# Kernel optimization log

Hardware: AMD Instinct MI355X
Metric: run time of the kernel (lower is better)

Reference implementation:

```python
import jax, jax.numpy as jnp
import numpy as np

B, A, D = 16384, 16, 256  # batch, n_different_edges (= attribute nodes), embedding_size


def setup_inputs() -> dict:
    key = jax.random.key(0)
    k0, k1, k2, k3, k4 = jax.random.split(key, 5)
    image_features = jax.random.normal(k0, (B, D), jnp.float32)
    edge_attributes = jax.random.normal(k1, (B, A, D), jnp.float32)
    # Linear(2D -> D): torch stores weight as [out, in]
    W_agg = jax.random.normal(k2, (D, 2 * D), jnp.float32) / np.sqrt(2 * D)
    b_agg = jnp.zeros((D,), jnp.float32)
    # per-edge-type projection matrices (kaiming-uniform in torch; scaled normal here)
    P_fwd = jax.random.normal(k3, (A, D, D), jnp.float32) * np.sqrt(2.0 / D)
    P_bwd = jax.random.normal(k4, (A, D, D), jnp.float32) * np.sqrt(2.0 / D)
    self_weighted = jnp.ones((1, A, 1), jnp.float32)
    return {
        "image_features": image_features,
        "edge_attributes": edge_attributes,
        "W_agg": W_agg,
        "b_agg": b_agg,
        "P_fwd": P_fwd,
        "P_bwd": P_bwd,
        "self_weighted": self_weighted,
    }


def reference(image_features, edge_attributes, W_agg, b_agg, P_fwd, P_bwd, self_weighted):
    b, a, d = edge_attributes.shape
    # ForwardAttributeGnn: broadcast src over attribute nodes, concat, Linear, per-edge-type bmm
    src = jnp.broadcast_to(image_features[:, None, :], (b, a, d))
    cat = jnp.concatenate([src, edge_attributes], axis=-1)          # [B, A, 2D]
    agg = jnp.einsum('bak,ok->bao', cat, W_agg) + b_agg             # Linear(2D->D)
    attribute_representation = jnp.einsum('bai,aij->baj', agg, P_fwd)  # [B, A, D]
    # BackwardAttributeGnn: per-edge-type bmm, ReLU, weighted sum over attribute axis
    proj = jax.nn.relu(jnp.einsum('bai,aij->baj', attribute_representation, P_bwd))
    individual_embeddings = jnp.sum(proj * self_weighted, axis=1)   # [B, D]
    return attribute_representation, individual_embeddings
```

## Files before the change

### kernel.cpp

```cpp
#include <hip/hip_runtime.h>
#include <hip/hip_bf16.h>


typedef __bf16 bf16_t;
typedef __bf16 bf16x4 __attribute__((ext_vector_type(4)));
typedef __bf16 bf16x8 __attribute__((ext_vector_type(8)));
typedef float f32x4 __attribute__((ext_vector_type(4)));

#define NB 16384
#define NA 16
#define ND 256
#define BM 64

__device__ __forceinline__ int swz(int r, int c) {
    return r * 256 + (c ^ ((r & 15) << 3));
}

__device__ __forceinline__ bf16x8 cvt8(f32x4 a, f32x4 b) {
    bf16x8 r;
    r[0] = (bf16_t)a.x; r[1] = (bf16_t)a.y; r[2] = (bf16_t)a.z; r[3] = (bf16_t)a.w;
    r[4] = (bf16_t)b.x; r[5] = (bf16_t)b.y; r[6] = (bf16_t)b.z; r[7] = (bf16_t)b.w;
    return r;
}

__global__ void prep_wfrag(const float* __restrict__ W,
                           bf16_t* __restrict__ W1f, bf16_t* __restrict__ W2f)
{
    int t = blockIdx.x * 256 + threadIdx.x;
    int lane = t & 63;
    int ks = (t >> 6) & 7;
    int nt = (t >> 9) & 15;
    int half = t >> 13;
    int row = nt * 16 + (lane & 15);
    int col = ks * 32 + (lane >> 4) * 8;
    const float* src = W + (size_t)row * 512 + half * 256 + col;
    bf16_t* dst = (half ? W2f : W1f) + ((nt * 8 + ks) * 64 + lane) * 8;
    bf16x8 v;
#pragma unroll
    for (int m = 0; m < 8; ++m) v[m] = (bf16_t)src[m];
    *(bf16x8*)dst = v;
}

__global__ void prep_pfrag2(const float* __restrict__ Pf, const float* __restrict__ Pb,
                            bf16_t* __restrict__ Pff, bf16_t* __restrict__ Pbf)
{
    int gw = (blockIdx.x * 256 + threadIdx.x) >> 6;
    int lane = threadIdx.x & 63;
    int frag = gw & 127;
    int a = (gw >> 7) & 15;
    int mat = gw >> 11;
    int nt = frag >> 3, ks = frag & 7;
    const float* src = (mat ? Pb : Pf) + (size_t)a * 65536;
    bf16_t* dst = (mat ? Pbf : Pff) + (size_t)a * 65536 + ((size_t)frag * 64 + lane) * 8;
    int i0 = ks * 32 + (lane >> 4) * 8;
    int j = nt * 16 + (lane & 15);
    bf16x8 v;
#pragma unroll
    for (int m = 0; m < 8; ++m)
        v[m] = (bf16_t)src[(size_t)(i0 + m) * 256 + j];
    *(bf16x8*)dst = v;
}

__global__ __launch_bounds__(512, 2)
void fused_main(const float* __restrict__ img, const float* __restrict__ bias,
                const float* __restrict__ edge,
                const bf16_t* __restrict__ W1f, const bf16_t* __restrict__ W2f,
                const bf16_t* __restrict__ Pff, const bf16_t* __restrict__ Pbf,
                const float* __restrict__ sw, float* __restrict__ out)
{
    __shared__ bf16_t EG[BM * 256];
    __shared__ bf16_t Rl[BM * 256];
    __shared__ float  Tl[BM * 256];

    const int tid = threadIdx.x;
    const int lane = tid & 63;
    const int wc = tid >> 6;
    const int lr = lane & 15;
    const int lhi = lane >> 4;
    const int brow0 = blockIdx.x * BM;
    const int sr = tid >> 3;
    const int scb = (tid & 7) * 32;

    bf16x8 B[2][8];

#define LOADB(MAT) do {                                                       \
    const bf16_t* bp_ = (MAT) + (size_t)wc * 16 * 512 + lane * 8;             \
    _Pragma("unroll") for (int ni_ = 0; ni_ < 2; ++ni_)                       \
    _Pragma("unroll") for (int ks_ = 0; ks_ < 8; ++ks_)                       \
        B[ni_][ks_] = *(const bf16x8*)&bp_[(ni_ * 8 + ks_) * 512];            \
} while (0)

#define SUBGEMM(SRC, IB, ACC) do {                                            \
    _Pragma("unroll") for (int ks_ = 0; ks_ < 8; ++ks_) {                     \
        const int kc_ = ks_ * 32 + lhi * 8;                                   \
        bf16x8 af0_ = *(const bf16x8*)&(SRC)[swz((IB) * 32 + lr, kc_)];       \
        bf16x8 af1_ = *(const bf16x8*)&(SRC)[swz((IB) * 32 + 16 + lr, kc_)];  \
        ACC[0][0] = __builtin_amdgcn_mfma_f32_16x16x32_bf16(af0_, B[0][ks_], ACC[0][0], 0, 0, 0); \
        ACC[1][0] = __builtin_amdgcn_mfma_f32_16x16x32_bf16(af1_, B[0][ks_], ACC[1][0], 0, 0, 0); \
        ACC[0][1] = __builtin_amdgcn_mfma_f32_16x16x32_bf16(af0_, B[1][ks_], ACC[0][1], 0, 0, 0); \
        ACC[1][1] = __builtin_amdgcn_mfma_f32_16x16x32_bf16(af1_, B[1][ks_], ACC[1][1], 0, 0, 0); \
    }                                                                         \
} while (0)

#define WRITEC(DST, IB, ACC) do {                                             \
    _Pragma("unroll") for (int mi_ = 0; mi_ < 2; ++mi_)                       \
    _Pragma("unroll") for (int ni_ = 0; ni_ < 2; ++ni_)                       \
    _Pragma("unroll") for (int j_ = 0; j_ < 4; ++j_)                          \
        (DST)[swz((IB) * 32 + mi_ * 16 + lhi * 4 + j_, wc * 32 + ni_ * 16 + lr)] = (bf16_t)ACC[mi_][ni_][j_]; \
} while (0)

#define STAGE_EDGE(A_) do {                                                   \
    const float* ep_ = edge + ((size_t)(brow0 + sr) * NA + (A_)) * ND + scb;  \
    f32x4 w0 = *(const f32x4*)(ep_ + 0),  w1 = *(const f32x4*)(ep_ + 4);      \
    f32x4 w2 = *(const f32x4*)(ep_ + 8),  w3 = *(const f32x4*)(ep_ + 12);     \
    f32x4 w4 = *(const f32x4*)(ep_ + 16), w5 = *(const f32x4*)(ep_ + 20);     \
    f32x4 w6 = *(const f32x4*)(ep_ + 24), w7 = *(const f32x4*)(ep_ + 28);     \
    *(bf16x8*)&EG[swz(sr, scb + 0)]  = cvt8(w0, w1);                          \
    *(bf16x8*)&EG[swz(sr, scb + 8)]  = cvt8(w2, w3);                          \
    *(bf16x8*)&EG[swz(sr, scb + 16)] = cvt8(w4, w5);                          \
    *(bf16x8*)&EG[swz(sr, scb + 24)] = cvt8(w6, w7);                          \
} while (0)

    {
        const float* ip = img + (size_t)(brow0 + sr) * ND + scb;
#pragma unroll
        for (int q = 0; q < 4; ++q) {
            f32x4 v0 = *(const f32x4*)(ip + q * 8);
            f32x4 v1 = *(const f32x4*)(ip + q * 8 + 4);
            *(bf16x8*)&EG[swz(sr, scb + q * 8)] = cvt8(v0, v1);
        }
    }
    __syncthreads();

    f32x4 acc0[2][2], acc1[2][2];
    {
        LOADB(W1f);
#pragma unroll
        for (int ni = 0; ni < 2; ++ni) {
            float bz = bias[wc * 32 + ni * 16 + lr];
            acc0[0][ni] = (f32x4){bz, bz, bz, bz}; acc0[1][ni] = (f32x4){bz, bz, bz, bz};
            acc1[0][ni] = (f32x4){bz, bz, bz, bz}; acc1[1][ni] = (f32x4){bz, bz, bz, bz};
        }
        SUBGEMM(EG, 0, acc0);
        SUBGEMM(EG, 1, acc1);
#pragma unroll
        for (int mi = 0; mi < 2; ++mi)
#pragma unroll
            for (int ni = 0; ni < 2; ++ni)
#pragma unroll
                for (int j = 0; j < 4; ++j) {
                    int c = wc * 32 + ni * 16 + lr;
                    Tl[(mi * 16 + lhi * 4 + j) * 256 + c] = acc0[mi][ni][j];
                    Tl[(32 + mi * 16 + lhi * 4 + j) * 256 + c] = acc1[mi][ni][j];
                }
    }
    __syncthreads();

    STAGE_EDGE(0);
    __syncthreads();

    f32x4 indiv[2][2][2];
#pragma unroll
    for (int i = 0; i < 2; ++i)
#pragma unroll
        for (int mi = 0; mi < 2; ++mi)
#pragma unroll
            for (int ni = 0; ni < 2; ++ni)
                indiv[i][mi][ni] = (f32x4){0.f, 0.f, 0.f, 0.f};

    for (int a = 0; a < NA; ++a) {
        LOADB(W2f);
#pragma unroll
        for (int mi = 0; mi < 2; ++mi)
#pragma unroll
            for (int ni = 0; ni < 2; ++ni)
#pragma unroll
                for (int j = 0; j < 4; ++j) {
                    int c = wc * 32 + ni * 16 + lr;
                    acc0[mi][ni][j] = Tl[(mi * 16 + lhi * 4 + j) * 256 + c];
                    acc1[mi][ni][j] = Tl[(32 + mi * 16 + lhi * 4 + j) * 256 + c];
                }
        SUBGEMM(EG, 0, acc0);
        SUBGEMM(EG, 1, acc1);
        __syncthreads();
        WRITEC(EG, 0, acc0);
        WRITEC(EG, 1, acc1);
        __syncthreads();

        LOADB(Pff + (size_t)a * 65536);
#pragma unroll
        for (int mi = 0; mi < 2; ++mi)
#pragma unroll
            for (int ni = 0; ni < 2; ++ni) {
                acc0[mi][ni] = (f32x4){0.f, 0.f, 0.f, 0.f};
                acc1[mi][ni] = (f32x4){0.f, 0.f, 0.f, 0.f};
            }
        SUBGEMM(EG, 0, acc0);
        SUBGEMM(EG, 1, acc1);
        WRITEC(Rl, 0, acc0);
        WRITEC(Rl, 1, acc1);
        __syncthreads();

        LOADB(Pbf + (size_t)a * 65536);
        {
            float* op = out + (size_t)(brow0 + sr) * (NA * ND) + (size_t)a * ND + scb;
#pragma unroll
            for (int q = 0; q < 4; ++q) {
                bf16x8 v = *(const bf16x8*)&Rl[swz(sr, scb + q * 8)];
                f32x4 lo = {(float)v[0], (float)v[1], (float)v[2], (float)v[3]};
                f32x4 hi = {(float)v[4], (float)v[5], (float)v[6], (float)v[7]};
                *(f32x4*)(op + q * 8) = lo;
                *(f32x4*)(op + q * 8 + 4) = hi;
            }
        }
#pragma unroll
        for (int mi = 0; mi < 2; ++mi)
#pragma unroll
            for (int ni = 0; ni < 2; ++ni) {
                acc0[mi][ni] = (f32x4){0.f, 0.f, 0.f, 0.f};
                acc1[mi][ni] = (f32x4){0.f, 0.f, 0.f, 0.f};
            }
        SUBGEMM(Rl, 0, acc0);
        SUBGEMM(Rl, 1, acc1);
        const float swa = sw[a];
#pragma unroll
        for (int mi = 0; mi < 2; ++mi)
#pragma unroll
            for (int ni = 0; ni < 2; ++ni)
#pragma unroll
                for (int j = 0; j < 4; ++j) {
                    indiv[0][mi][ni][j] += fmaxf(acc0[mi][ni][j], 0.f) * swa;
                    indiv[1][mi][ni][j] += fmaxf(acc1[mi][ni][j], 0.f) * swa;
                }
        if (a + 1 < NA) {
            STAGE_EDGE(a + 1);
        }
        __syncthreads();
    }

#pragma unroll
    for (int i = 0; i < 2; ++i)
#pragma unroll
        for (int mi = 0; mi < 2; ++mi)
#pragma unroll
            for (int ni = 0; ni < 2; ++ni)
#pragma unroll
                for (int j = 0; j < 4; ++j) {
                    int r = i * 32 + mi * 16 + lhi * 4 + j;
                    int c = wc * 32 + ni * 16 + lr;
                    out[(size_t)NB * NA * ND + (size_t)(brow0 + r) * ND + c] = indiv[i][mi][ni][j];
                }
#undef LOADB
#undef SUBGEMM
#undef WRITEC
#undef STAGE_EDGE
}

extern "C" void kernel_launch(void* const* d_in, const int* in_sizes, int n_in,
                              void* d_out, int out_size, void* d_ws, size_t ws_size,
                              hipStream_t stream)
{
    const float* img  = (const float*)d_in[0];
    const float* edge = (const float*)d_in[1];
    const float* Wagg = (const float*)d_in[2];
    const float* bagg = (const float*)d_in[3];
    const float* Pf   = (const float*)d_in[4];
    const float* Pb   = (const float*)d_in[5];
    const float* sw   = (const float*)d_in[6];
    float* out = (float*)d_out;

    char* ws = (char*)d_ws;
    bf16_t* W1f = (bf16_t*)(ws);
    bf16_t* W2f = (bf16_t*)(ws + 131072);
    bf16_t* Pff = (bf16_t*)(ws + 262144);
    bf16_t* Pbf = (bf16_t*)(ws + 2359296);

    prep_wfrag<<<64, 256, 0, stream>>>(Wagg, W1f, W2f);
    prep_pfrag2<<<1024, 256, 0, stream>>>(Pf, Pb, Pff, Pbf);
    fused_main<<<NB / BM, 512, 0, stream>>>(img, bagg, edge, W1f, W2f, Pff, Pbf, sw, out);
}
```

Before: 304.5 us.

## Double-buffer B fragments and LDS tiles to prefetch next weights and drop barriers

Uses two register sets for the B-operand fragments so the next matrix (Pff, Pbf, W2f) is loaded while the current GEMM runs. Ping-pongs two LDS buffers so the W2 output can go to the other buffer without an extra barrier. Processes one 32-row half at a time with a single accumulator set to cut register pressure. The cost is a second B register set, which may spill or lower occupancy at launch_bounds(512,2).

```diff
diff --git a/kernel.cpp b/kernel.cpp
--- a/kernel.cpp
+++ b/kernel.cpp
@@ -68,8 +68,8 @@
                 const bf16_t* __restrict__ Pff, const bf16_t* __restrict__ Pbf,
                 const float* __restrict__ sw, float* __restrict__ out)
 {
-    __shared__ bf16_t EG[BM * 256];
-    __shared__ bf16_t Rl[BM * 256];
+    __shared__ bf16_t Xb[BM * 256];
+    __shared__ bf16_t Yb[BM * 256];
     __shared__ float  Tl[BM * 256];
 
     const int tid = threadIdx.x;
@@ -81,44 +81,102 @@
     const int sr = tid >> 3;
     const int scb = (tid & 7) * 32;
 
-    bf16x8 B[2][8];
-
-#define LOADB(MAT) do {                                                       \
+    bf16x8 BA[2][8], BB[2][8];
+    f32x4 acc[2][2];
+    f32x4 indiv[2][2][2];
+
+#define LOADB_TO(BSET, MAT) do {                                              \
     const bf16_t* bp_ = (MAT) + (size_t)wc * 16 * 512 + lane * 8;             \
     _Pragma("unroll") for (int ni_ = 0; ni_ < 2; ++ni_)                       \
     _Pragma("unroll") for (int ks_ = 0; ks_ < 8; ++ks_)                       \
-        B[ni_][ks_] = *(const bf16x8*)&bp_[(ni_ * 8 + ks_) * 512];            \
-} while (0)
-
-#define SUBGEMM(SRC, IB, ACC) do {                                            \
+        BSET[ni_][ks_] = *(const bf16x8*)&bp_[(ni_ * 8 + ks_) * 512];         \
+} while (0)
+
+#define SUBGEMM_B(SRC, IB, BSET) do {                                         \
     _Pragma("unroll") for (int ks_ = 0; ks_ < 8; ++ks_) {                     \
         const int kc_ = ks_ * 32 + lhi * 8;                                   \
         bf16x8 af0_ = *(const bf16x8*)&(SRC)[swz((IB) * 32 + lr, kc_)];       \
         bf16x8 af1_ = *(const bf16x8*)&(SRC)[swz((IB) * 32 + 16 + lr, kc_)];  \
-        ACC[0][0] = __builtin_amdgcn_mfma_f32_16x16x32_bf16(af0_, B[0][ks_], ACC[0][0], 0, 0, 0); \
-        ACC[1][0] = __builtin_amdgcn_mfma_f32_16x16x32_bf16(af1_, B[0][ks_], ACC[1][0], 0, 0, 0); \
-        ACC[0][1] = __builtin_amdgcn_mfma_f32_16x16x32_bf16(af0_, B[1][ks_], ACC[0][1], 0, 0, 0); \
-        ACC[1][1] = __builtin_amdgcn_mfma_f32_16x16x32_bf16(af1_, B[1][ks_], ACC[1][1], 0, 0, 0); \
-    }                                                                         \
-} while (0)
-
-#define WRITEC(DST, IB, ACC) do {                                             \
+        acc[0][0] = __builtin_amdgcn_mfma_f32_16x16x32_bf16(af0_, BSET[0][ks_], acc[0][0], 0, 0, 0); \
+        acc[1][0] = __builtin_amdgcn_mfma_f32_16x16x32_bf16(af1_, BSET[0][ks_], acc[1][0], 0, 0, 0); \
+        acc[0][1] = __builtin_amdgcn_mfma_f32_16x16x32_bf16(af0_, BSET[1][ks_], acc[0][1], 0, 0, 0); \
+        acc[1][1] = __builtin_amdgcn_mfma_f32_16x16x32_bf16(af1_, BSET[1][ks_], acc[1][1], 0, 0, 0); \
+    }                                                                         \
+} while (0)
+
+#define WRITEC(DST, IB) do {                                                  \
     _Pragma("unroll") for (int mi_ = 0; mi_ < 2; ++mi_)                       \
     _Pragma("unroll") for (int ni_ = 0; ni_ < 2; ++ni_)                       \
     _Pragma("unroll") for (int j_ = 0; j_ < 4; ++j_)                          \
-        (DST)[swz((IB) * 32 + mi_ * 16 + lhi * 4 + j_, wc * 32 + ni_ * 16 + lr)] = (bf16_t)ACC[mi_][ni_][j_]; \
-} while (0)
-
-#define STAGE_EDGE(A_) do {                                                   \
+        (DST)[swz((IB) * 32 + mi_ * 16 + lhi * 4 + j_, wc * 32 + ni_ * 16 + lr)] = (bf16_t)acc[mi_][ni_][j_]; \
+} while (0)
+
+#define ACC_FROM_T(IB) do {                                                   \
+    _Pragma("unroll") for (int mi_ = 0; mi_ < 2; ++mi_)                       \
+    _Pragma("unroll") for (int ni_ = 0; ni_ < 2; ++ni_)                       \
+    _Pragma("unroll") for (int j_ = 0; j_ < 4; ++j_)                          \
+        acc[mi_][ni_][j_] = Tl[((IB) * 32 + mi_ * 16 + lhi * 4 + j_) * 256 + wc * 32 + ni_ * 16 + lr]; \
+} while (0)
+
+#define ACC_ZERO() do {                                                       \
+    _Pragma("unroll") for (int mi_ = 0; mi_ < 2; ++mi_)                       \
+    _Pragma("unroll") for (int ni_ = 0; ni_ < 2; ++ni_)                       \
+        acc[mi_][ni_] = (f32x4){0.f, 0.f, 0.f, 0.f};                          \
+} while (0)
+
+#define STAGE_EDGE_TO(DST, A_) do {                                           \
     const float* ep_ = edge + ((size_t)(brow0 + sr) * NA + (A_)) * ND + scb;  \
     f32x4 w0 = *(const f32x4*)(ep_ + 0),  w1 = *(const f32x4*)(ep_ + 4);      \
     f32x4 w2 = *(const f32x4*)(ep_ + 8),  w3 = *(const f32x4*)(ep_ + 12);     \
     f32x4 w4 = *(const f32x4*)(ep_ + 16), w5 = *(const f32x4*)(ep_ + 20);     \
     f32x4 w6 = *(const f32x4*)(ep_ + 24), w7 = *(const f32x4*)(ep_ + 28);     \
-    *(bf16x8*)&EG[swz(sr, scb + 0)]  = cvt8(w0, w1);                          \
-    *(bf16x8*)&EG[swz(sr, scb + 8)]  = cvt8(w2, w3);                          \
-    *(bf16x8*)&EG[swz(sr, scb + 16)] = cvt8(w4, w5);                          \
-    *(bf16x8*)&EG[swz(sr, scb + 24)] = cvt8(w6, w7);                          \
+    *(bf16x8*)&(DST)[swz(sr, scb + 0)]  = cvt8(w0, w1);                       \
+    *(bf16x8*)&(DST)[swz(sr, scb + 8)]  = cvt8(w2, w3);                       \
+    *(bf16x8*)&(DST)[swz(sr, scb + 16)] = cvt8(w4, w5);                       \
+    *(bf16x8*)&(DST)[swz(sr, scb + 24)] = cvt8(w6, w7);                       \
+} while (0)
+
+#define ATTR_STORE(SRCBUF, A_) do {                                           \
+    float* op_ = out + (size_t)(brow0 + sr) * (NA * ND) + (size_t)(A_) * ND + scb; \
+    _Pragma("unroll") for (int q_ = 0; q_ < 4; ++q_) {                        \
+        bf16x8 v_ = *(const bf16x8*)&(SRCBUF)[swz(sr, scb + q_ * 8)];         \
+        f32x4 lo_ = {(float)v_[0], (float)v_[1], (float)v_[2], (float)v_[3]}; \
+        f32x4 hi_ = {(float)v_[4], (float)v_[5], (float)v_[6], (float)v_[7]}; \
+        *(f32x4*)(op_ + q_ * 8) = lo_;                                        \
+        *(f32x4*)(op_ + q_ * 8 + 4) = hi_;                                    \
+    }                                                                         \
+} while (0)
+
+#define ITER(A_, S, T_, EB, OB) do {                                          \
+                      \
+    LOADB_TO(T_, Pff + (size_t)(A_) * 65536);                                 \
+    ACC_FROM_T(0); SUBGEMM_B(EB, 0, S); WRITEC(OB, 0);                        \
+    ACC_FROM_T(1); SUBGEMM_B(EB, 1, S); WRITEC(OB, 1);                        \
+    __syncthreads();                                                          \
+                               \
+    LOADB_TO(S, Pbf + (size_t)(A_) * 65536);                                  \
+    ACC_ZERO(); SUBGEMM_B(OB, 0, T_); WRITEC(EB, 0);                          \
+    ACC_ZERO(); SUBGEMM_B(OB, 1, T_); WRITEC(EB, 1);                          \
+    __syncthreads();                                                          \
+                                                \
+    if ((A_) + 1 < NA) LOADB_TO(T_, W2f);                                     \
+    ATTR_STORE(EB, A_);                                                       \
+    ACC_ZERO(); SUBGEMM_B(EB, 0, S);                                          \
+    {   const float swa_ = sw[A_];                                            \
+        _Pragma("unroll") for (int mi_ = 0; mi_ < 2; ++mi_)                   \
+        _Pragma("unroll") for (int ni_ = 0; ni_ < 2; ++ni_)                   \
+        _Pragma("unroll") for (int j_ = 0; j_ < 4; ++j_)                      \
+            indiv[0][mi_][ni_][j_] += fmaxf(acc[mi_][ni_][j_], 0.f) * swa_;   \
+    }                                                                         \
+    ACC_ZERO(); SUBGEMM_B(EB, 1, S);                                          \
+    {   const float swa_ = sw[A_];                                            \
+        _Pragma("unroll") for (int mi_ = 0; mi_ < 2; ++mi_)                   \
+        _Pragma("unroll") for (int ni_ = 0; ni_ < 2; ++ni_)                   \
+        _Pragma("unroll") for (int j_ = 0; j_ < 4; ++j_)                      \
+            indiv[1][mi_][ni_][j_] += fmaxf(acc[mi_][ni_][j_], 0.f) * swa_;   \
+    }                                                                         \
+    if ((A_) + 1 < NA) STAGE_EDGE_TO(OB, (A_) + 1);                           \
+    __syncthreads();                                                          \
 } while (0)
 
     {
@@ -127,39 +185,38 @@
         for (int q = 0; q < 4; ++q) {
             f32x4 v0 = *(const f32x4*)(ip + q * 8);
             f32x4 v1 = *(const f32x4*)(ip + q * 8 + 4);
-            *(bf16x8*)&EG[swz(sr, scb + q * 8)] = cvt8(v0, v1);
+            *(bf16x8*)&Xb[swz(sr, scb + q * 8)] = cvt8(v0, v1);
         }
     }
     __syncthreads();
 
-    f32x4 acc0[2][2], acc1[2][2];
+    LOADB_TO(BA, W1f);
     {
-        LOADB(W1f);
-#pragma unroll
-        for (int ni = 0; ni < 2; ++ni) {
-            float bz = bias[wc * 32 + ni * 16 + lr];
-            acc0[0][ni] = (f32x4){bz, bz, bz, bz}; acc0[1][ni] = (f32x4){bz, bz, bz, bz};
-            acc1[0][ni] = (f32x4){bz, bz, bz, bz}; acc1[1][ni] = (f32x4){bz, bz, bz, bz};
+        float bz0 = bias[wc * 32 + lr];
+        float bz1 = bias[wc * 32 + 16 + lr];
+#pragma unroll
+        for (int ib = 0; ib < 2; ++ib) {
+            acc[0][0] = (f32x4){bz0, bz0, bz0, bz0};
+            acc[1][0] = (f32x4){bz0, bz0, bz0, bz0};
+            acc[0][1] = (f32x4){bz1, bz1, bz1, bz1};
+            acc[1][1] = (f32x4){bz1, bz1, bz1, bz1};
+            if (ib == 0) { SUBGEMM_B(Xb, 0, BA); }
+            else         { SUBGEMM_B(Xb, 1, BA); }
+#pragma unroll
+            for (int mi = 0; mi < 2; ++mi)
+#pragma unroll
+                for (int ni = 0; ni < 2; ++ni)
+#pragma unroll
+                    for (int j = 0; j < 4; ++j)
+                        Tl[(ib * 32 + mi * 16 + lhi * 4 + j) * 256 + wc * 32 + ni * 16 + lr] = acc[mi][ni][j];
         }
-        SUBGEMM(EG, 0, acc0);
-        SUBGEMM(EG, 1, acc1);
-#pragma unroll
-        for (int mi = 0; mi < 2; ++mi)
-#pragma unroll
-            for (int ni = 0; ni < 2; ++ni)
-#pragma unroll
-                for (int j = 0; j < 4; ++j) {
-                    int c = wc * 32 + ni * 16 + lr;
-                    Tl[(mi * 16 + lhi * 4 + j) * 256 + c] = acc0[mi][ni][j];
-                    Tl[(32 + mi * 16 + lhi * 4 + j) * 256 + c] = acc1[mi][ni][j];
-                }
     }
     __syncthreads();
 
-    STAGE_EDGE(0);
+    STAGE_EDGE_TO(Xb, 0);
+    LOADB_TO(BA, W2f);
     __syncthreads();
 
-    f32x4 indiv[2][2][2];
 #pragma unroll
     for (int i = 0; i < 2; ++i)
 #pragma unroll
@@ -168,74 +225,10 @@
             for (int ni = 0; ni < 2; ++ni)
                 indiv[i][mi][ni] = (f32x4){0.f, 0.f, 0.f, 0.f};
 
-    for (int a = 0; a < NA; ++a) {
-        LOADB(W2f);
-#pragma unroll
-        for (int mi = 0; mi < 2; ++mi)
-#pragma unroll
-            for (int ni = 0; ni < 2; ++ni)
-#pragma unroll
-                for (int j = 0; j < 4; ++j) {
-                    int c = wc * 32 + ni * 16 + lr;
-                    acc0[mi][ni][j] = Tl[(mi * 16 + lhi * 4 + j) * 256 + c];
-                    acc1[mi][ni][j] = Tl[(32 + mi * 16 + lhi * 4 + j) * 256 + c];
-                }
-        SUBGEMM(EG, 0, acc0);
-        SUBGEMM(EG, 1, acc1);
-        __syncthreads();
-        WRITEC(EG, 0, acc0);
-        WRITEC(EG, 1, acc1);
-        __syncthreads();
-
-        LOADB(Pff + (size_t)a * 65536);
-#pragma unroll
-        for (int mi = 0; mi < 2; ++mi)
-#pragma unroll
-            for (int ni = 0; ni < 2; ++ni) {
-                acc0[mi][ni] = (f32x4){0.f, 0.f, 0.f, 0.f};
-                acc1[mi][ni] = (f32x4){0.f, 0.f, 0.f, 0.f};
-            }
-        SUBGEMM(EG, 0, acc0);
-        SUBGEMM(EG, 1, acc1);
-        WRITEC(Rl, 0, acc0);
-        WRITEC(Rl, 1, acc1);
-        __syncthreads();
-
-        LOADB(Pbf + (size_t)a * 65536);
-        {
-            float* op = out + (size_t)(brow0 + sr) * (NA * ND) + (size_t)a * ND + scb;
-#pragma unroll
-            for (int q = 0; q < 4; ++q) {
-                bf16x8 v = *(const bf16x8*)&Rl[swz(sr, scb + q * 8)];
-                f32x4 lo = {(float)v[0], (float)v[1], (float)v[2], (float)v[3]};
-                f32x4 hi = {(float)v[4], (float)v[5], (float)v[6], (float)v[7]};
-                *(f32x4*)(op + q * 8) = lo;
-                *(f32x4*)(op + q * 8 + 4) = hi;
-            }
-        }
-#pragma unroll
-        for (int mi = 0; mi < 2; ++mi)
-#pragma unroll
-            for (int ni = 0; ni < 2; ++ni) {
-                acc0[mi][ni] = (f32x4){0.f, 0.f, 0.f, 0.f};
-                acc1[mi][ni] = (f32x4){0.f, 0.f, 0.f, 0.f};
-            }
-        SUBGEMM(Rl, 0, acc0);
-        SUBGEMM(Rl, 1, acc1);
-        const float swa = sw[a];
-#pragma unroll
-        for (int mi = 0; mi < 2; ++mi)
-#pragma unroll
-            for (int ni = 0; ni < 2; ++ni)
-#pragma unroll
-                for (int j = 0; j < 4; ++j) {
-                    indiv[0][mi][ni][j] += fmaxf(acc0[mi][ni][j], 0.f) * swa;
-                    indiv[1][mi][ni][j] += fmaxf(acc1[mi][ni][j], 0.f) * swa;
-                }
-        if (a + 1 < NA) {
-            STAGE_EDGE(a + 1);
-        }
-        __syncthreads();
+    for (int ah = 0; ah < 8; ++ah) {
+        const int a0 = ah * 2;
+        ITER(a0,     BA, BB, Xb, Yb);
+        ITER(a0 + 1, BB, BA, Yb, Xb);
     }
 
 #pragma unroll
@@ -250,10 +243,14 @@
                     int c = wc * 32 + ni * 16 + lr;
                     out[(size_t)NB * NA * ND + (size_t)(brow0 + r) * ND + c] = indiv[i][mi][ni][j];
                 }
-#undef LOADB
-#undef SUBGEMM
+#undef LOADB_TO
+#undef SUBGEMM_B
 #undef WRITEC
-#undef STAGE_EDGE
+#undef ACC_FROM_T
+#undef ACC_ZERO
+#undef STAGE_EDGE_TO
+#undef ATTR_STORE
+#undef ITER
 }
 
 extern "C" void kernel_launch(void* const* d_in, const int* in_sizes, int n_in,
```

New measurement: 407.5 us. 33.8% more time.
